# Kernel optimization log

Hardware: AMD Instinct MI355X
Metric: run time of the kernel (lower is better)

The kernel has to match this reference:

```python
import jax, jax.numpy as jnp
import numpy as np

EMB = 1024
HEADS = 16
HEAD_DIM = EMB // HEADS
B, T = 2, 2048
EPS = 1e-5


def setup_inputs() -> dict:
    key = jax.random.key(0)
    ks = jax.random.split(key, 12)
    s_in = (1.0 / np.sqrt(EMB)).astype(np.float32)
    s_hid = (1.0 / np.sqrt(4 * EMB)).astype(np.float32)
    return {
        "x": jax.random.normal(ks[0], (B, T, EMB), jnp.float32),
        "Wq": jax.random.normal(ks[1], (HEADS, EMB, HEAD_DIM), jnp.float32) * s_in,
        "Wk": jax.random.normal(ks[2], (HEADS, EMB, HEAD_DIM), jnp.float32) * s_in,
        "Wv": jax.random.normal(ks[3], (HEADS, EMB, HEAD_DIM), jnp.float32) * s_in,
        "W1": jax.random.normal(ks[4], (EMB, 4 * EMB), jnp.float32) * s_in,
        "b1": jnp.zeros((4 * EMB,), jnp.float32),
        "W2": jax.random.normal(ks[5], (4 * EMB, EMB), jnp.float32) * s_hid,
        "b2": jnp.zeros((EMB,), jnp.float32),
        "g1": jnp.ones((EMB,), jnp.float32),
        "be1": jnp.zeros((EMB,), jnp.float32),
        "g2": jnp.ones((EMB,), jnp.float32),
        "be2": jnp.zeros((EMB,), jnp.float32),
    }


def _layernorm1d(x, gain, bias):
    # Faithful to source: normalize over dim 1 (sequence dim of [B,T,C]),
    # with UNBIASED variance (torch.var default).
    mean = jnp.mean(x, axis=1, keepdims=True)
    var = jnp.var(x, axis=1, keepdims=True, ddof=1)
    return gain * (x - mean) / jnp.sqrt(var + EPS) + bias


def _attention(x, Wq, Wk, Wv):
    Bq, Tq, C = x.shape
    q = jnp.einsum("btc,hcd->bhtd", x, Wq)
    k = jnp.einsum("btc,hcd->bhtd", x, Wk)
    v = jnp.einsum("btc,hcd->bhtd", x, Wv)
    # NOTE: scale uses input channel dim C (=emb_size), as in the source.
    wei = jnp.einsum("bhtd,bhsd->bhts", q, k) * (C ** -0.5)
    causal = jnp.tril(jnp.ones((Tq, Tq), bool))
    wei = jnp.where(causal, wei, -jnp.inf)
    wei = jax.nn.softmax(wei, axis=-1)
    out = jnp.einsum("bhts,bhsd->bhtd", wei, v)
    # concat over heads (dim=-1) == transpose + reshape
    return out.transpose(0, 2, 1, 3).reshape(Bq, Tq, -1)


def reference(x, Wq, Wk, Wv, W1, b1, W2, b2, g1, be1, g2, be2):
    x = x + _attention(_layernorm1d(x, g1, be1), Wq, Wk, Wv)
    h = _layernorm1d(x, g2, be2)
    h = jax.nn.relu(h @ W1 + b1) @ W2 + b2
    return x + h
```

## Files before the change

### kernel.cpp

```cpp
#include <hip/hip_runtime.h>


typedef __bf16 bf16x8 __attribute__((ext_vector_type(8)));
typedef float f32x4 __attribute__((ext_vector_type(4)));
typedef unsigned short u16;
typedef u16 u16x8 __attribute__((ext_vector_type(8)));
typedef u16 u16x4 __attribute__((ext_vector_type(4)));

#define MFMA16 __builtin_amdgcn_mfma_f32_16x16x32_bf16

__device__ __forceinline__ u16 f2bf(float f) {
  return __builtin_bit_cast(u16, (__bf16)f);
}
__device__ __forceinline__ float bf2f(u16 u) {
  return __builtin_bit_cast(float, (unsigned)u << 16);
}
__device__ __forceinline__ bf16x8 ldbf8(const u16* p) {
  return __builtin_bit_cast(bf16x8, *reinterpret_cast<const u16x8*>(p));
}
__device__ __forceinline__ void gll16(const void* g, void* l) {
  __builtin_amdgcn_global_load_lds((const __attribute__((address_space(1))) void*)g,
                                   (__attribute__((address_space(3))) void*)l, 16, 0, 0);
}
template <int N>
__device__ __forceinline__ void wait_vm() {
  if constexpr (N == 0)      asm volatile("s_waitcnt vmcnt(0)" ::: "memory");
  else if constexpr (N == 2) asm volatile("s_waitcnt vmcnt(2)" ::: "memory");
  else if constexpr (N == 6) asm volatile("s_waitcnt vmcnt(6)" ::: "memory");
  else if constexpr (N == 8) asm volatile("s_waitcnt vmcnt(8)" ::: "memory");
  else                       asm volatile("s_waitcnt vmcnt(16)" ::: "memory");
}
__device__ __forceinline__ void barrier_raw() {
  asm volatile("" ::: "memory");
  __builtin_amdgcn_s_barrier();
  asm volatile("" ::: "memory");
}
__device__ __forceinline__ int qb_off(int qb) {
  if (qb < 8)  return qb;
  if (qb < 16) return 8 + (qb - 8) * 2;
  if (qb < 24) return 24 + (qb - 16) * 3;
  return 48 + (qb - 24) * 4;
}

__global__ __launch_bounds__(256) void transpose_big(const float* __restrict__ in,
                                                     u16* __restrict__ out, int K, int N) {
  __shared__ float tile[64][65];
  const int k0 = blockIdx.x * 64, n0 = blockIdx.y * 64;
  const int c = threadIdx.x & 63, rg = threadIdx.x >> 6;
#pragma unroll
  for (int i = 0; i < 16; ++i) {
    int r = rg * 16 + i;
    tile[r][c] = in[(size_t)(k0 + r) * N + n0 + c];
  }
  __syncthreads();
#pragma unroll
  for (int i = 0; i < 16; ++i) {
    int nl = rg * 16 + i;
    out[(size_t)(n0 + nl) * K + k0 + c] = f2bf(tile[c][nl]);
  }
}

__global__ __launch_bounds__(256) void transpose_head3(const float* __restrict__ Wq,
                                                       const float* __restrict__ Wk,
                                                       const float* __restrict__ Wv,
                                                       u16* __restrict__ out, float scale) {
  __shared__ float tile[64][65];
  const int z = blockIdx.z;
  const float* W = z == 0 ? Wq : (z == 1 ? Wk : Wv);
  const float sc = z == 0 ? scale : 1.0f;
  const int k0 = blockIdx.x * 64, h = blockIdx.y;
  const float* in = W + (size_t)h * 1024 * 64;
  const int c = threadIdx.x & 63, rg = threadIdx.x >> 6;
#pragma unroll
  for (int i = 0; i < 16; ++i) {
    int r = rg * 16 + i;
    tile[r][c] = in[(size_t)(k0 + r) * 64 + c];
  }
  __syncthreads();
#pragma unroll
  for (int i = 0; i < 16; ++i) {
    int nl = rg * 16 + i;
    out[(size_t)(z * 1024 + h * 64 + nl) * 1024 + k0 + c] = f2bf(tile[c][nl] * sc);
  }
}

__global__ __launch_bounds__(256) void ln_partial(const float* __restrict__ x,
                                                  float2* __restrict__ part) {
  const int b = blockIdx.x >> 4, c0 = (blockIdx.x & 15) * 64;
  const int c = c0 + (threadIdx.x & 63), tg = threadIdx.x >> 6;
  const int t0 = blockIdx.y * 256 + tg * 64;
  float s = 0.f, sq = 0.f;
  const float* p = x + (size_t)(b * 2048 + t0) * 1024 + c;
#pragma unroll 8
  for (int i = 0; i < 64; ++i) {
    float v = p[(size_t)i * 1024];
    s += v; sq += v * v;
  }
  __shared__ float ss[256], sb[256];
  ss[threadIdx.x] = s; sb[threadIdx.x] = sq;
  __syncthreads();
  if (threadIdx.x < 64) {
    s  = ss[threadIdx.x] + ss[threadIdx.x + 64] + ss[threadIdx.x + 128] + ss[threadIdx.x + 192];
    sq = sb[threadIdx.x] + sb[threadIdx.x + 64] + sb[threadIdx.x + 128] + sb[threadIdx.x + 192];
    part[(size_t)(b * 1024 + c) * 8 + blockIdx.y] = make_float2(s, sq);
  }
}

__global__ __launch_bounds__(256) void ln_stats(const float2* __restrict__ part,
                                                float2* __restrict__ stats) {
  const int bc = blockIdx.x * 256 + threadIdx.x;
  float s = 0.f, sq = 0.f;
#pragma unroll
  for (int i = 0; i < 8; ++i) {
    float2 v = part[(size_t)bc * 8 + i];
    s += v.x; sq += v.y;
  }
  const float mean = s * (1.0f / 2048.0f);
  const float var = (sq - 2048.0f * mean * mean) * (1.0f / 2047.0f);
  stats[bc] = make_float2(mean, rsqrtf(var + 1e-5f));
}

__global__ __launch_bounds__(256) void ln_apply(const float* __restrict__ x,
                                                const float2* __restrict__ stats,
                                                const float* __restrict__ g,
                                                const float* __restrict__ be,
                                                u16* __restrict__ out) {
  const size_t flat = ((size_t)blockIdx.x * 256 + threadIdx.x) * 4;
  const int b = (int)(flat >> 21);
  const int c = (int)(flat & 1023);
  float4 xv = *reinterpret_cast<const float4*>(x + flat);
  float vs[4] = {xv.x, xv.y, xv.z, xv.w};
  u16x4 o;
#pragma unroll
  for (int j = 0; j < 4; ++j) {
    float2 st = stats[b * 1024 + c + j];
    o[j] = f2bf(g[c + j] * (vs[j] - st.x) * st.y + be[c + j]);
  }
  *reinterpret_cast<u16x4*>(out + flat) = o;
}

template <int WTN, int EPI, int MINW>
__global__ __launch_bounds__(256, MINW) void gemm_kernel(const u16* __restrict__ A,
                                                         const u16* __restrict__ Bt,
                                                         u16* __restrict__ outb,
                                                         float* __restrict__ outf,
                                                         const float* __restrict__ bias,
                                                         const float* __restrict__ resid,
                                                         int N, int K) {
  constexpr int BM = 128, BN = 2 * WTN;
  constexpr int NI = WTN / 16;
  constexpr int BCH = BN / 8;
  constexpr int LPW = (16 + BCH) / 4;
  __shared__ alignas(16) u16 sA[2][BM * 64];
  __shared__ alignas(16) u16 sB[2][BN * 64];
  const int gx = gridDim.x;
  const int nwg = gx * gridDim.y;
  int bid = blockIdx.y * gx + blockIdx.x;
  bid = (bid & 7) * (nwg >> 3) + (bid >> 3);
  const int n0 = (bid % gx) * BN, m0 = (bid / gx) * BM;
  const int tid = threadIdx.x, lane = tid & 63, wid = tid >> 6;
  const int wm = (wid >> 1) * 64, wn = (wid & 1) * WTN;
  const int lr = lane & 15, lg = lane >> 4;
  const int srow = lane >> 3;
  const int sgr = (lane & 7) ^ srow;
  const int x7 = lr & 7;
  f32x4 acc[4][NI] = {};

  auto stage = [&](int buf, int k0) {
#pragma unroll
    for (int i = 0; i < LPW; ++i) {
      const int c = wid * LPW + i;
      if (c < 16) {
        const int r = c * 8 + srow;
        gll16(A + (size_t)(m0 + r) * K + k0 + sgr * 8, &sA[buf][c * 512]);
      } else {
        const int r = (c - 16) * 8 + srow;
        gll16(Bt + (size_t)(n0 + r) * K + k0 + sgr * 8, &sB[buf][(c - 16) * 512]);
      }
    }
  };

  const int nsteps = K >> 6;
  stage(0, 0);
  int cur = 0;
  for (int t = 0; t < nsteps; ++t) {
    if (t + 1 < nsteps) {
      stage(cur ^ 1, (t + 1) * 64);
      wait_vm<LPW>();
    } else {
      wait_vm<0>();
    }
    barrier_raw();
    bf16x8 af[4][2], bfr[NI][2];
#pragma unroll
    for (int mi = 0; mi < 4; ++mi)
#pragma unroll
      for (int kk = 0; kk < 2; ++kk)
        af[mi][kk] = ldbf8(&sA[cur][(wm + mi * 16 + lr) * 64 + (((kk * 4 + lg) ^ x7) * 8)]);
#pragma unroll
    for (int ni = 0; ni < NI; ++ni)
#pragma unroll
      for (int kk = 0; kk < 2; ++kk)
        bfr[ni][kk] = ldbf8(&sB[cur][(wn + ni * 16 + lr) * 64 + (((kk * 4 + lg) ^ x7) * 8)]);
#pragma unroll
    for (int kk = 0; kk < 2; ++kk)
#pragma unroll
      for (int mi = 0; mi < 4; ++mi)
#pragma unroll
        for (int ni = 0; ni < NI; ++ni)
          acc[mi][ni] = MFMA16(af[mi][kk], bfr[ni][kk], acc[mi][ni], 0, 0, 0);
    barrier_raw();
    cur ^= 1;
  }

#pragma unroll
  for (int mi = 0; mi < 4; ++mi)
#pragma unroll
    for (int ni = 0; ni < NI; ++ni)
#pragma unroll
      for (int r = 0; r < 4; ++r) {
        const int row = m0 + wm + mi * 16 + lg * 4 + r;
        const int col = n0 + wn + ni * 16 + lr;
        float v = acc[mi][ni][r];
        if (EPI == 0) {
          outb[(size_t)row * N + col] = f2bf(v);
        } else if (EPI == 1) {
          v += bias[col];
          v = fmaxf(v, 0.f);
          outb[(size_t)row * N + col] = f2bf(v);
        } else {
          v += bias[col] + resid[(size_t)row * N + col];
          outf[(size_t)row * N + col] = v;
        }
      }
}

__global__ __launch_bounds__(512, 6) void attn_partial(const u16* __restrict__ qk,
                                                       const u16* __restrict__ vt,
                                                       u16* __restrict__ Opart,
                                                       float2* __restrict__ ml) {
  const int xr = 39 - (int)blockIdx.x;
  int j, i;
  if (xr < 16)      { j = 0; i = xr; }
  else if (xr < 28) { j = 1; i = xr - 16; }
  else if (xr < 36) { j = 2; i = xr - 28; }
  else              { j = 3; i = xr - 36; }
  const int qb1 = j * 8 + 2 * i;
  const int bh = blockIdx.y, b = bh >> 4, h = bh & 15;
  const int tid = threadIdx.x, lane = tid & 63, w = tid >> 6;
  const int qsel = w >> 2, wl = w & 3;
  const int qb = qb1 + qsel;
  const int lr = lane & 15, lg = lane >> 4;
  const int t_lo = 8 * j;
  const int t_hi_raw = 8 * (j + 1);
  const int t_hi = (qb1 + 2 < t_hi_raw) ? qb1 + 2 : t_hi_raw;
  __shared__ alignas(16) u16 sK[2][64 * 64];
  __shared__ alignas(16) u16 sV[2][64 * 64];
  __shared__ alignas(16) u16 sP[8][16 * 64];

  const size_t qrow = (size_t)(b * 2048 + qb * 64 + wl * 16 + lr) * 2048 + h * 64;
  const bf16x8 aq0 = ldbf8(qk + qrow + lg * 8);
  const bf16x8 aq1 = ldbf8(qk + qrow + 32 + lg * 8);

  float m_i[4], l_i[4];
  f32x4 acc[4];
#pragma unroll
  for (int r = 0; r < 4; ++r) { m_i[r] = -1e30f; l_i[r] = 0.f; }
#pragma unroll
  for (int dn = 0; dn < 4; ++dn) acc[dn] = f32x4{0.f, 0.f, 0.f, 0.f};

  auto stage = [&](int buf, int s0) {
    const int g = w * 64 + lane;
    const int row = g >> 3;
    const int cs = (g & 7) ^ (row & 7);
    gll16(qk + (size_t)(b * 2048 + s0 + row) * 2048 + 1024 + h * 64 + cs * 8,
          &sK[buf][w * 512]);
    gll16(vt + (size_t)(h * 64 + row) * 4096 + b * 2048 + s0 + cs * 8,
          &sV[buf][w * 512]);
  };

  stage(0, t_lo * 64);

  for (int t = t_lo; t < t_hi; ++t) {
    const int buf = (t - t_lo) & 1;
    if (t + 1 < t_hi) {
      stage(buf ^ 1, (t + 1) * 64);
      wait_vm<2>();
    } else {
      wait_vm<0>();
    }
    barrier_raw();

    if (t <= qb) {
      const u16* Kb = sK[buf];
      const u16* Vb = sV[buf];
      f32x4 sf[4];
      __builtin_amdgcn_s_setprio(1);
#pragma unroll
      for (int sn = 0; sn < 4; ++sn) {
        const int row = sn * 16 + lr;
        const int x7 = lr & 7;
        bf16x8 k0f = ldbf8(&Kb[row * 64 + ((lg ^ x7) * 8)]);
        bf16x8 k1f = ldbf8(&Kb[row * 64 + (((4 + lg) ^ x7) * 8)]);
        f32x4 z = {0.f, 0.f, 0.f, 0.f};
        z = MFMA16(aq0, k0f, z, 0, 0, 0);
        z = MFMA16(aq1, k1f, z, 0, 0, 0);
        sf[sn] = z;
      }
      __builtin_amdgcn_s_setprio(0);

      if (t == qb) {
        const int qlb = wl * 16 + lg * 4;
#pragma unroll
        for (int sn = 0; sn < 4; ++sn)
#pragma unroll
          for (int r = 0; r < 4; ++r)
            if (sn * 16 + lr > qlb + r) sf[sn][r] = -1e30f;
      }

      float pm[4];
      bool need = false;
#pragma unroll
      for (int r = 0; r < 4; ++r) {
        pm[r] = fmaxf(fmaxf(sf[0][r], sf[1][r]), fmaxf(sf[2][r], sf[3][r]));
        need = need || (pm[r] > m_i[r] + 8.f);
      }
      if (__any(need)) {
#pragma unroll
        for (int r = 0; r < 4; ++r) {
          float mx = pm[r];
          mx = fmaxf(mx, __shfl_xor(mx, 1, 16));
          mx = fmaxf(mx, __shfl_xor(mx, 2, 16));
          mx = fmaxf(mx, __shfl_xor(mx, 4, 16));
          mx = fmaxf(mx, __shfl_xor(mx, 8, 16));
          const float mnew = fmaxf(m_i[r], mx);
          const float al = exp2f(m_i[r] - mnew);
          l_i[r] *= al;
          acc[0][r] *= al; acc[1][r] *= al; acc[2][r] *= al; acc[3][r] *= al;
          m_i[r] = mnew;
        }
      }

      const int x7p = lr & 7;
#pragma unroll
      for (int r = 0; r < 4; ++r) {
        const float p0 = exp2f(sf[0][r] - m_i[r]), p1 = exp2f(sf[1][r] - m_i[r]);
        const float p2 = exp2f(sf[2][r] - m_i[r]), p3 = exp2f(sf[3][r] - m_i[r]);
        l_i[r] += (p0 + p1) + (p2 + p3);
        const int prow = lg * 4 + r;
        const int pb = prow * 64, px = prow & 7;
        sP[w][pb + (((lr >> 3) ^ px) * 8) + (lr & 7)]       = f2bf(p0);
        sP[w][pb + (((2 + (lr >> 3)) ^ px) * 8) + (lr & 7)] = f2bf(p1);
        sP[w][pb + (((4 + (lr >> 3)) ^ px) * 8) + (lr & 7)] = f2bf(p2);
        sP[w][pb + (((6 + (lr >> 3)) ^ px) * 8) + (lr & 7)] = f2bf(p3);
      }

      const bf16x8 pa0 = ldbf8(&sP[w][lr * 64 + ((lg ^ x7p) * 8)]);
      const bf16x8 pa1 = ldbf8(&sP[w][lr * 64 + (((4 + lg) ^ x7p) * 8)]);
      __builtin_amdgcn_s_setprio(1);
#pragma unroll
      for (int dn = 0; dn < 4; ++dn) {
        const int row = dn * 16 + lr;
        bf16x8 v0f = ldbf8(&Vb[row * 64 + ((lg ^ x7p) * 8)]);
        bf16x8 v1f = ldbf8(&Vb[row * 64 + (((4 + lg) ^ x7p) * 8)]);
        acc[dn] = MFMA16(pa0, v0f, acc[dn], 0, 0, 0);
        acc[dn] = MFMA16(pa1, v1f, acc[dn], 0, 0, 0);
      }
      __builtin_amdgcn_s_setprio(0);
    }
    barrier_raw();
  }

  const int slot = bh * 80 + qb_off(qb) + j;
  const int rbase = wl * 16 + lg * 4;
#pragma unroll
  for (int r = 0; r < 4; ++r) {
    float ls = l_i[r];
    ls += __shfl_xor(ls, 1, 16);
    ls += __shfl_xor(ls, 2, 16);
    ls += __shfl_xor(ls, 4, 16);
    ls += __shfl_xor(ls, 8, 16);
    const int row = rbase + r;
    if (lr == 0) ml[(size_t)slot * 64 + row] = make_float2(m_i[r], ls);
#pragma unroll
    for (int dn = 0; dn < 4; ++dn)
      Opart[((size_t)slot * 64 + row) * 64 + dn * 16 + lr] = f2bf(acc[dn][r]);
  }
}

__global__ __launch_bounds__(256) void attn_merge(const u16* __restrict__ Opart,
                                                  const float2* __restrict__ ml,
                                                  const float* __restrict__ x,
                                                  float* __restrict__ x2) {
  const int qb = blockIdx.x, bh = blockIdx.y, b = bh >> 4, h = bh & 15;
  const int nc = (qb >> 3) + 1;
  const size_t slot0 = (size_t)bh * 80 + qb_off(qb);
  const int tid = threadIdx.x;
  const int row = tid >> 2, d0 = (tid & 3) * 16;

  float wgt[4];
  float mmax = -1e30f, lsum = 0.f;
  for (int i = 0; i < nc; ++i) {
    float2 v = ml[(slot0 + i) * 64 + row];
    wgt[i] = v.x;
    mmax = fmaxf(mmax, v.x);
  }
  for (int i = 0; i < nc; ++i) {
    float2 v = ml[(slot0 + i) * 64 + row];
    wgt[i] = exp2f(wgt[i] - mmax);
    lsum += wgt[i] * v.y;
  }
  const float inv = 1.0f / lsum;

#pragma unroll
  for (int half = 0; half < 2; ++half) {
    const int d = d0 + half * 8;
    float o[8] = {0.f, 0.f, 0.f, 0.f, 0.f, 0.f, 0.f, 0.f};
    for (int i = 0; i < nc; ++i) {
      u16x8 v = *reinterpret_cast<const u16x8*>(&Opart[((slot0 + i) * 64 + row) * 64 + d]);
#pragma unroll
      for (int jj = 0; jj < 8; ++jj) o[jj] += wgt[i] * bf2f(v[jj]);
    }
    const size_t idx = ((size_t)(b * 2048 + qb * 64 + row)) * 1024 + h * 64 + d;
    float4 x0 = *reinterpret_cast<const float4*>(x + idx);
    float4 x1 = *reinterpret_cast<const float4*>(x + idx + 4);
    float4 o0 = make_float4(x0.x + o[0] * inv, x0.y + o[1] * inv, x0.z + o[2] * inv, x0.w + o[3] * inv);
    float4 o1 = make_float4(x1.x + o[4] * inv, x1.y + o[5] * inv, x1.z + o[6] * inv, x1.w + o[7] * inv);
    *reinterpret_cast<float4*>(x2 + idx) = o0;
    *reinterpret_cast<float4*>(x2 + idx + 4) = o1;
  }
}

extern "C" void kernel_launch(void* const* d_in, const int* in_sizes, int n_in,
                              void* d_out, int out_size, void* d_ws, size_t ws_size,
                              hipStream_t stream) {
  const float* x   = (const float*)d_in[0];
  const float* Wq  = (const float*)d_in[1];
  const float* Wk  = (const float*)d_in[2];
  const float* Wv  = (const float*)d_in[3];
  const float* W1  = (const float*)d_in[4];
  const float* b1  = (const float*)d_in[5];
  const float* W2  = (const float*)d_in[6];
  const float* b2  = (const float*)d_in[7];
  const float* g1  = (const float*)d_in[8];
  const float* be1 = (const float*)d_in[9];
  const float* g2  = (const float*)d_in[10];
  const float* be2 = (const float*)d_in[11];
  float* out = (float*)d_out;

  char* ws = (char*)d_ws;
  size_t off = 0;
  auto alloc = [&](size_t bytes) { char* p = ws + off; off += (bytes + 255) & ~(size_t)255; return p; };
  u16*    qkb   = (u16*)alloc(4096ull * 2048 * 2);
  u16*    vtb   = (u16*)alloc(1024ull * 4096 * 2);
  (void)alloc(4096ull * 1024 * 2);
  u16*    h1    = qkb;
  float*  x2    = (float*)alloc(4096ull * 1024 * 4);
  u16*    hbuf  = (u16*)alloc(4096ull * 1024 * 2);
  u16*    wqkvt = (u16*)alloc(3072ull * 1024 * 2);
  u16*    w1t   = (u16*)alloc(4096ull * 1024 * 2);
  u16*    w2t   = (u16*)alloc(1024ull * 4096 * 2);
  float2* part  = (float2*)alloc(2048ull * 8 * 8);
  float2* stats = (float2*)alloc(2048ull * 8);
  u16*    Opart = (u16*)alloc(32ull * 80 * 64 * 64 * 2);
  float2* ml    = (float2*)alloc(32ull * 80 * 64 * 8);
  (void)ws_size; (void)in_sizes; (void)n_in; (void)out_size;

  const float SC = 0.03125f * 1.44269504088896341f;
  transpose_head3<<<dim3(16, 16, 3), 256, 0, stream>>>(Wq, Wk, Wv, wqkvt, SC);
  transpose_big<<<dim3(16, 64), 256, 0, stream>>>(W1, w1t, 1024, 4096);
  transpose_big<<<dim3(64, 16), 256, 0, stream>>>(W2, w2t, 4096, 1024);

  ln_partial<<<dim3(32, 8), 256, 0, stream>>>(x, part);
  ln_stats<<<8, 256, 0, stream>>>(part, stats);
  ln_apply<<<4096, 256, 0, stream>>>(x, stats, g1, be1, hbuf);

  gemm_kernel<64, 0, 2><<<dim3(16, 32), 256, 0, stream>>>(hbuf, wqkvt, qkb, nullptr, nullptr, nullptr, 2048, 1024);
  gemm_kernel<32, 0, 3><<<dim3(64, 8), 256, 0, stream>>>(wqkvt + 2048 * 1024, hbuf, vtb, nullptr, nullptr, nullptr, 4096, 1024);

  attn_partial<<<dim3(40, 32), 512, 0, stream>>>(qkb, vtb, Opart, ml);
  attn_merge<<<dim3(32, 32), 256, 0, stream>>>(Opart, ml, x, x2);

  ln_partial<<<dim3(32, 8), 256, 0, stream>>>(x2, part);
  ln_stats<<<8, 256, 0, stream>>>(part, stats);
  ln_apply<<<4096, 256, 0, stream>>>(x2, stats, g2, be2, hbuf);

  gemm_kernel<64, 1, 2><<<dim3(32, 32), 256, 0, stream>>>(hbuf, w1t, h1, nullptr, b1, nullptr, 4096, 1024);

  gemm_kernel<32, 2, 3><<<dim3(16, 32), 256, 0, stream>>>(h1, w2t, nullptr, out, b2, x2, 1024, 4096);
}
```

Baseline: 268.7 us.

## Split attention work per query block into balanced KV chunks with 256-thread blocks

Attention partial kernel now assigns one 64-row query block per 256-thread workgroup and splits its causal KV range into 1-4 even chunks, launching 80x32 blocks instead of 40x32 paired-query blocks. This removes the idle iterations where one of two paired query blocks skipped tiles (t > qb), and balances the work per block. Each block now stages K/V with two loads per thread and waits on vmcnt(4). The trade-off is more blocks, with each K/V tile feeding only one query block, so K/V loads are reused less.

```diff
diff --git a/kernel.cpp b/kernel.cpp
--- a/kernel.cpp
+++ b/kernel.cpp
@@ -25,7 +25,7 @@
 template <int N>
 __device__ __forceinline__ void wait_vm() {
   if constexpr (N == 0)      asm volatile("s_waitcnt vmcnt(0)" ::: "memory");
-  else if constexpr (N == 2) asm volatile("s_waitcnt vmcnt(2)" ::: "memory");
+  else if constexpr (N == 4) asm volatile("s_waitcnt vmcnt(4)" ::: "memory");
   else if constexpr (N == 6) asm volatile("s_waitcnt vmcnt(6)" ::: "memory");
   else if constexpr (N == 8) asm volatile("s_waitcnt vmcnt(8)" ::: "memory");
   else                       asm volatile("s_waitcnt vmcnt(16)" ::: "memory");
@@ -235,30 +235,29 @@
       }
 }
 
-__global__ __launch_bounds__(512, 6) void attn_partial(const u16* __restrict__ qk,
-                                                       const u16* __restrict__ vt,
-                                                       u16* __restrict__ Opart,
-                                                       float2* __restrict__ ml) {
-  const int xr = 39 - (int)blockIdx.x;
-  int j, i;
-  if (xr < 16)      { j = 0; i = xr; }
-  else if (xr < 28) { j = 1; i = xr - 16; }
-  else if (xr < 36) { j = 2; i = xr - 28; }
-  else              { j = 3; i = xr - 36; }
-  const int qb1 = j * 8 + 2 * i;
+__global__ __launch_bounds__(256) void attn_partial(const u16* __restrict__ qk,
+                                                    const u16* __restrict__ vt,
+                                                    u16* __restrict__ Opart,
+                                                    float2* __restrict__ ml) {
+  const int xr = 79 - (int)blockIdx.x;
+  int qb, ch, nc;
+  if (xr < 8)       { qb = xr;                ch = 0;            nc = 1; }
+  else if (xr < 24) { qb = 8 + ((xr - 8) >> 1);  ch = (xr - 8) & 1;  nc = 2; }
+  else if (xr < 48) { qb = 16 + (xr - 24) / 3;   ch = (xr - 24) % 3; nc = 3; }
+  else              { qb = 24 + ((xr - 48) >> 2); ch = (xr - 48) & 3; nc = 4; }
+  const int nt_tot = qb + 1;
+  const int t0 = (ch * nt_tot) / nc;
+  const int t1 = ((ch + 1) * nt_tot) / nc;
   const int bh = blockIdx.y, b = bh >> 4, h = bh & 15;
+  const int slot = bh * 80 + xr;
+  const int q0 = qb * 64;
   const int tid = threadIdx.x, lane = tid & 63, w = tid >> 6;
-  const int qsel = w >> 2, wl = w & 3;
-  const int qb = qb1 + qsel;
   const int lr = lane & 15, lg = lane >> 4;
-  const int t_lo = 8 * j;
-  const int t_hi_raw = 8 * (j + 1);
-  const int t_hi = (qb1 + 2 < t_hi_raw) ? qb1 + 2 : t_hi_raw;
   __shared__ alignas(16) u16 sK[2][64 * 64];
   __shared__ alignas(16) u16 sV[2][64 * 64];
-  __shared__ alignas(16) u16 sP[8][16 * 64];
-
-  const size_t qrow = (size_t)(b * 2048 + qb * 64 + wl * 16 + lr) * 2048 + h * 64;
+  __shared__ alignas(16) u16 sP[4][16 * 64];
+
+  const size_t qrow = (size_t)(b * 2048 + q0 + w * 16 + lr) * 2048 + h * 64;
   const bf16x8 aq0 = ldbf8(qk + qrow + lg * 8);
   const bf16x8 aq1 = ldbf8(qk + qrow + 32 + lg * 8);
 
@@ -270,109 +269,110 @@
   for (int dn = 0; dn < 4; ++dn) acc[dn] = f32x4{0.f, 0.f, 0.f, 0.f};
 
   auto stage = [&](int buf, int s0) {
-    const int g = w * 64 + lane;
-    const int row = g >> 3;
-    const int cs = (g & 7) ^ (row & 7);
-    gll16(qk + (size_t)(b * 2048 + s0 + row) * 2048 + 1024 + h * 64 + cs * 8,
-          &sK[buf][w * 512]);
-    gll16(vt + (size_t)(h * 64 + row) * 4096 + b * 2048 + s0 + cs * 8,
-          &sV[buf][w * 512]);
+#pragma unroll
+    for (int i = 0; i < 2; ++i) {
+      const int c = w * 2 + i;
+      const int g = c * 64 + lane;
+      const int row = g >> 3;
+      const int cs = (g & 7) ^ (row & 7);
+      gll16(qk + (size_t)(b * 2048 + s0 + row) * 2048 + 1024 + h * 64 + cs * 8,
+            &sK[buf][c * 512]);
+      gll16(vt + (size_t)(h * 64 + row) * 4096 + b * 2048 + s0 + cs * 8,
+            &sV[buf][c * 512]);
+    }
   };
 
-  stage(0, t_lo * 64);
-
-  for (int t = t_lo; t < t_hi; ++t) {
-    const int buf = (t - t_lo) & 1;
-    if (t + 1 < t_hi) {
+  stage(0, t0 * 64);
+
+  for (int t = t0; t < t1; ++t) {
+    const int buf = (t - t0) & 1;
+    if (t + 1 < t1) {
       stage(buf ^ 1, (t + 1) * 64);
-      wait_vm<2>();
+      wait_vm<4>();
     } else {
       wait_vm<0>();
     }
     barrier_raw();
 
-    if (t <= qb) {
-      const u16* Kb = sK[buf];
-      const u16* Vb = sV[buf];
-      f32x4 sf[4];
-      __builtin_amdgcn_s_setprio(1);
-#pragma unroll
-      for (int sn = 0; sn < 4; ++sn) {
-        const int row = sn * 16 + lr;
-        const int x7 = lr & 7;
-        bf16x8 k0f = ldbf8(&Kb[row * 64 + ((lg ^ x7) * 8)]);
-        bf16x8 k1f = ldbf8(&Kb[row * 64 + (((4 + lg) ^ x7) * 8)]);
-        f32x4 z = {0.f, 0.f, 0.f, 0.f};
-        z = MFMA16(aq0, k0f, z, 0, 0, 0);
-        z = MFMA16(aq1, k1f, z, 0, 0, 0);
-        sf[sn] = z;
+    const u16* Kb = sK[buf];
+    const u16* Vb = sV[buf];
+    f32x4 sf[4];
+    __builtin_amdgcn_s_setprio(1);
+#pragma unroll
+    for (int sn = 0; sn < 4; ++sn) {
+      const int row = sn * 16 + lr;
+      const int x7 = lr & 7;
+      bf16x8 k0f = ldbf8(&Kb[row * 64 + ((lg ^ x7) * 8)]);
+      bf16x8 k1f = ldbf8(&Kb[row * 64 + (((4 + lg) ^ x7) * 8)]);
+      f32x4 z = {0.f, 0.f, 0.f, 0.f};
+      z = MFMA16(aq0, k0f, z, 0, 0, 0);
+      z = MFMA16(aq1, k1f, z, 0, 0, 0);
+      sf[sn] = z;
+    }
+    __builtin_amdgcn_s_setprio(0);
+
+    if (t == nt_tot - 1) {
+      const int qlb = w * 16 + lg * 4;
+#pragma unroll
+      for (int sn = 0; sn < 4; ++sn)
+#pragma unroll
+        for (int r = 0; r < 4; ++r)
+          if (sn * 16 + lr > qlb + r) sf[sn][r] = -1e30f;
+    }
+
+    float pm[4];
+    bool need = false;
+#pragma unroll
+    for (int r = 0; r < 4; ++r) {
+      pm[r] = fmaxf(fmaxf(sf[0][r], sf[1][r]), fmaxf(sf[2][r], sf[3][r]));
+      need = need || (pm[r] > m_i[r] + 8.f);
+    }
+    if (__any(need)) {
+#pragma unroll
+      for (int r = 0; r < 4; ++r) {
+        float mx = pm[r];
+        mx = fmaxf(mx, __shfl_xor(mx, 1, 16));
+        mx = fmaxf(mx, __shfl_xor(mx, 2, 16));
+        mx = fmaxf(mx, __shfl_xor(mx, 4, 16));
+        mx = fmaxf(mx, __shfl_xor(mx, 8, 16));
+        const float mnew = fmaxf(m_i[r], mx);
+        const float al = exp2f(m_i[r] - mnew);
+        l_i[r] *= al;
+        acc[0][r] *= al; acc[1][r] *= al; acc[2][r] *= al; acc[3][r] *= al;
+        m_i[r] = mnew;
       }
-      __builtin_amdgcn_s_setprio(0);
-
-      if (t == qb) {
-        const int qlb = wl * 16 + lg * 4;
-#pragma unroll
-        for (int sn = 0; sn < 4; ++sn)
-#pragma unroll
-          for (int r = 0; r < 4; ++r)
-            if (sn * 16 + lr > qlb + r) sf[sn][r] = -1e30f;
-      }
-
-      float pm[4];
-      bool need = false;
-#pragma unroll
-      for (int r = 0; r < 4; ++r) {
-        pm[r] = fmaxf(fmaxf(sf[0][r], sf[1][r]), fmaxf(sf[2][r], sf[3][r]));
-        need = need || (pm[r] > m_i[r] + 8.f);
-      }
-      if (__any(need)) {
-#pragma unroll
-        for (int r = 0; r < 4; ++r) {
-          float mx = pm[r];
-          mx = fmaxf(mx, __shfl_xor(mx, 1, 16));
-          mx = fmaxf(mx, __shfl_xor(mx, 2, 16));
-          mx = fmaxf(mx, __shfl_xor(mx, 4, 16));
-          mx = fmaxf(mx, __shfl_xor(mx, 8, 16));
-          const float mnew = fmaxf(m_i[r], mx);
-          const float al = exp2f(m_i[r] - mnew);
-          l_i[r] *= al;
-          acc[0][r] *= al; acc[1][r] *= al; acc[2][r] *= al; acc[3][r] *= al;
-          m_i[r] = mnew;
-        }
-      }
-
-      const int x7p = lr & 7;
-#pragma unroll
-      for (int r = 0; r < 4; ++r) {
-        const float p0 = exp2f(sf[0][r] - m_i[r]), p1 = exp2f(sf[1][r] - m_i[r]);
-        const float p2 = exp2f(sf[2][r] - m_i[r]), p3 = exp2f(sf[3][r] - m_i[r]);
-        l_i[r] += (p0 + p1) + (p2 + p3);
-        const int prow = lg * 4 + r;
-        const int pb = prow * 64, px = prow & 7;
-        sP[w][pb + (((lr >> 3) ^ px) * 8) + (lr & 7)]       = f2bf(p0);
-        sP[w][pb + (((2 + (lr >> 3)) ^ px) * 8) + (lr & 7)] = f2bf(p1);
-        sP[w][pb + (((4 + (lr >> 3)) ^ px) * 8) + (lr & 7)] = f2bf(p2);
-        sP[w][pb + (((6 + (lr >> 3)) ^ px) * 8) + (lr & 7)] = f2bf(p3);
-      }
-
-      const bf16x8 pa0 = ldbf8(&sP[w][lr * 64 + ((lg ^ x7p) * 8)]);
-      const bf16x8 pa1 = ldbf8(&sP[w][lr * 64 + (((4 + lg) ^ x7p) * 8)]);
-      __builtin_amdgcn_s_setprio(1);
-#pragma unroll
-      for (int dn = 0; dn < 4; ++dn) {
-        const int row = dn * 16 + lr;
-        bf16x8 v0f = ldbf8(&Vb[row * 64 + ((lg ^ x7p) * 8)]);
-        bf16x8 v1f = ldbf8(&Vb[row * 64 + (((4 + lg) ^ x7p) * 8)]);
-        acc[dn] = MFMA16(pa0, v0f, acc[dn], 0, 0, 0);
-        acc[dn] = MFMA16(pa1, v1f, acc[dn], 0, 0, 0);
-      }
-      __builtin_amdgcn_s_setprio(0);
-    }
+    }
+
+    const int x7p = lr & 7;
+#pragma unroll
+    for (int r = 0; r < 4; ++r) {
+      const float p0 = exp2f(sf[0][r] - m_i[r]), p1 = exp2f(sf[1][r] - m_i[r]);
+      const float p2 = exp2f(sf[2][r] - m_i[r]), p3 = exp2f(sf[3][r] - m_i[r]);
+      l_i[r] += (p0 + p1) + (p2 + p3);
+      const int prow = lg * 4 + r;
+      const int pb = prow * 64, px = prow & 7;
+      sP[w][pb + (((lr >> 3) ^ px) * 8) + (lr & 7)]       = f2bf(p0);
+      sP[w][pb + (((2 + (lr >> 3)) ^ px) * 8) + (lr & 7)] = f2bf(p1);
+      sP[w][pb + (((4 + (lr >> 3)) ^ px) * 8) + (lr & 7)] = f2bf(p2);
+      sP[w][pb + (((6 + (lr >> 3)) ^ px) * 8) + (lr & 7)] = f2bf(p3);
+    }
+
+    const bf16x8 pa0 = ldbf8(&sP[w][lr * 64 + ((lg ^ x7p) * 8)]);
+    const bf16x8 pa1 = ldbf8(&sP[w][lr * 64 + (((4 + lg) ^ x7p) * 8)]);
+    __builtin_amdgcn_s_setprio(1);
+#pragma unroll
+    for (int dn = 0; dn < 4; ++dn) {
+      const int row = dn * 16 + lr;
+      bf16x8 v0f = ldbf8(&Vb[row * 64 + ((lg ^ x7p) * 8)]);
+      bf16x8 v1f = ldbf8(&Vb[row * 64 + (((4 + lg) ^ x7p) * 8)]);
+      acc[dn] = MFMA16(pa0, v0f, acc[dn], 0, 0, 0);
+      acc[dn] = MFMA16(pa1, v1f, acc[dn], 0, 0, 0);
+    }
+    __builtin_amdgcn_s_setprio(0);
     barrier_raw();
   }
 
-  const int slot = bh * 80 + qb_off(qb) + j;
-  const int rbase = wl * 16 + lg * 4;
+  const int rbase = w * 16 + lg * 4;
 #pragma unroll
   for (int r = 0; r < 4; ++r) {
     float ls = l_i[r];
@@ -478,7 +478,7 @@
   gemm_kernel<64, 0, 2><<<dim3(16, 32), 256, 0, stream>>>(hbuf, wqkvt, qkb, nullptr, nullptr, nullptr, 2048, 1024);
   gemm_kernel<32, 0, 3><<<dim3(64, 8), 256, 0, stream>>>(wqkvt + 2048 * 1024, hbuf, vtb, nullptr, nullptr, nullptr, 4096, 1024);
 
-  attn_partial<<<dim3(40, 32), 512, 0, stream>>>(qkb, vtb, Opart, ml);
+  attn_partial<<<dim3(80, 32), 256, 0, stream>>>(qkb, vtb, Opart, ml);
   attn_merge<<<dim3(32, 32), 256, 0, stream>>>(Opart, ml, x, x2);
 
   ln_partial<<<dim3(32, 8), 256, 0, stream>>>(x2, part);
```

Measured after the change: 248.5 us. -7.5%, faster.
